# Kernel tuning notes

Hardware: AMD Instinct MI355X
Metric: run time of the kernel (lower is better)

Reference implementation:

```python
import jax, jax.numpy as jnp
import numpy as np

N_HEADS = 16


def setup_inputs() -> dict:
    key = jax.random.key(0)
    ks = jax.random.split(key, 9)
    B, T, C, S = 32, 8, 1024, 4096
    w_scale = 1.0 / np.sqrt(C).astype(np.float32)
    return {
        "x": jax.random.normal(ks[0], (B, T, C), jnp.float32),
        "cache_k": jax.random.normal(ks[1], (B, S, C), jnp.float32),
        "cache_v": jax.random.normal(ks[2], (B, S, C), jnp.float32),
        "cache_len": jax.random.randint(ks[3], (B,), 0, S - T, jnp.int32),
        "wq": jax.random.normal(ks[4], (C, C), jnp.float32) * w_scale,
        "wk": jax.random.normal(ks[5], (C, C), jnp.float32) * w_scale,
        "wv": jax.random.normal(ks[6], (C, C), jnp.float32) * w_scale,
        "wo": jax.random.normal(ks[7], (C, C), jnp.float32) * w_scale,
        "bo": jnp.zeros((C,), jnp.float32),
    }


def reference(x, cache_k, cache_v, cache_len, wq, wk, wv, wo, bo):
    # Decode step with KV cache (use_cache=True, window_size=None, mask=None).
    B, T, C = x.shape
    S = cache_k.shape[1]  # max_seq_len (static pad; torch pads to max(cache_len))
    H = N_HEADS
    hd = C // H

    # Projections (torch Linear: y = x @ W^T)
    q = x @ wq.T
    k_new = x @ wk.T
    v_new = x @ wv.T

    # Ragged past-KV gather: zero-pad each row beyond its cache_len,
    # exactly like the per-batch loop + padded_k/padded_v in torch.
    pos = jnp.arange(S)
    past_mask = (pos[None, :] < cache_len[:, None])[..., None]  # (B, S, 1)
    past_k = jnp.where(past_mask, cache_k, 0.0)
    past_v = jnp.where(past_mask, cache_v, 0.0)

    k = jnp.concatenate([past_k, k_new], axis=1)  # (B, S+T, C)
    v = jnp.concatenate([past_v, v_new], axis=1)

    def to_heads(t):
        return t.reshape(B, t.shape[1], H, hd).transpose(0, 2, 1, 3)

    qh, kh, vh = to_heads(q), to_heads(k), to_heads(v)  # (B,H,*,hd)

    scores = jnp.einsum('bhqd,bhkd->bhqk', qh, kh) / np.sqrt(hd).astype(np.float32)

    # Torch only materializes keys up to max(cache_len); slots beyond that
    # do not exist there, so mask them out. Slots in [cache_len_b, max_cl)
    # are zero-padded keys (score 0, value 0) in torch -> kept as-is here.
    max_cl = jnp.max(cache_len)
    key_valid = jnp.concatenate([pos < max_cl, jnp.ones((T,), bool)])  # (S+T,)
    NEG = jnp.float32(-1e30)
    scores = jnp.where(key_valid[None, None, None, :], scores, NEG)

    attn = jax.nn.softmax(scores, axis=-1)
    out = jnp.einsum('bhqk,bhkd->bhqd', attn, vh)
    out = out.transpose(0, 2, 1, 3).reshape(B, T, C)
    return out @ wo.T + bo
```

## Files before the change

### kernel.cpp

```cpp
#include <hip/hip_runtime.h>

constexpr int Bn = 32, Tn = 8, Cn = 1024, Sn = 4096, Hn = 16, HDn = 64;
constexpr int CHUNK = 64, NCHUNK = 64;
constexpr int KSPLIT = 4;
constexpr float SCALE = 0.125f;

constexpr size_t PROJ_PART = (size_t)Bn * Tn * Cn;
constexpr size_t QP_OFF = 0;
constexpr size_t KP_OFF = QP_OFF + KSPLIT * PROJ_PART;
constexpr size_t VP_OFF = KP_OFF + KSPLIT * PROJ_PART;
constexpr size_t PACC_OFF = VP_OFF + KSPLIT * PROJ_PART;
constexpr size_t PACC_SZ = (size_t)NCHUNK * Bn * Hn * Tn * HDn;
constexpr size_t PL_OFF = PACC_OFF + PACC_SZ;
constexpr size_t PL_SZ = (size_t)NCHUNK * Bn * Hn * Tn;
constexpr size_t AW_OFF = PL_OFF + PL_SZ;
constexpr size_t AW_SZ = PROJ_PART;
constexpr size_t OP_OFF = AW_OFF + AW_SZ;
constexpr size_t OP_SZ = (size_t)KSPLIT * PROJ_PART;
constexpr size_t QR_OFF = OP_OFF + OP_SZ;
constexpr size_t KN_OFF = QR_OFF + PROJ_PART;
constexpr size_t VN_OFF = KN_OFF + PROJ_PART;

typedef __attribute__((address_space(3))) unsigned int lds_uint;
typedef const __attribute__((address_space(1))) unsigned int glb_uint;

__device__ __forceinline__ void gload_lds16(const float* g, float* l) {
    __builtin_amdgcn_global_load_lds((glb_uint*)g, (lds_uint*)l, 16, 0, 0);
}

__device__ __forceinline__ void gemm_body(const float* __restrict__ X,
                                          const float* __restrict__ W,
                                          float* __restrict__ Opart,
                                          int sigma, int jblk, int iblk) {
    __shared__ float wl[64][68];
    const int tid = threadIdx.x;
    const int c = tid & 15, a = tid >> 4;
    const int j0 = jblk * 64;
    const int ib = iblk * 64 + a * 4;
    const int k0 = sigma * 256;

    float acc[4][4];
#pragma unroll
    for (int ii = 0; ii < 4; ++ii)
#pragma unroll
        for (int jj = 0; jj < 4; ++jj) acc[ii][jj] = 0.f;

    for (int kt = 0; kt < 4; ++kt) {
        const int k1 = k0 + kt * 64;
#pragma unroll
        for (int stp = 0; stp < 4; ++stp) {
            int f4 = stp * 256 + tid;
            int jr = f4 >> 4, e4 = f4 & 15;
            float4 wv = *(const float4*)&W[(size_t)(j0 + jr) * Cn + k1 + e4 * 4];
            wl[e4 * 4 + 0][jr] = wv.x;
            wl[e4 * 4 + 1][jr] = wv.y;
            wl[e4 * 4 + 2][jr] = wv.z;
            wl[e4 * 4 + 3][jr] = wv.w;
        }
        __syncthreads();
#pragma unroll 4
        for (int k4 = 0; k4 < 16; ++k4) {
            float4 xv[4];
#pragma unroll
            for (int ii = 0; ii < 4; ++ii)
                xv[ii] = *(const float4*)&X[(size_t)(ib + ii) * Cn + k1 + k4 * 4];
#pragma unroll
            for (int kk = 0; kk < 4; ++kk) {
                float4 wv = *(const float4*)&wl[k4 * 4 + kk][c * 4];
#pragma unroll
                for (int ii = 0; ii < 4; ++ii) {
                    const float xs = (kk == 0) ? xv[ii].x : (kk == 1) ? xv[ii].y
                                   : (kk == 2) ? xv[ii].z : xv[ii].w;
                    acc[ii][0] += xs * wv.x;
                    acc[ii][1] += xs * wv.y;
                    acc[ii][2] += xs * wv.z;
                    acc[ii][3] += xs * wv.w;
                }
            }
        }
        __syncthreads();
    }
    float* op = Opart + (size_t)sigma * PROJ_PART;
#pragma unroll
    for (int ii = 0; ii < 4; ++ii) {
        float4 o = make_float4(acc[ii][0], acc[ii][1], acc[ii][2], acc[ii][3]);
        *(float4*)&op[(size_t)(ib + ii) * Cn + j0 + c * 4] = o;
    }
}

__global__ __launch_bounds__(256) void proj3_kernel(
    const float* __restrict__ X, const float* __restrict__ W0,
    const float* __restrict__ W1, const float* __restrict__ W2,
    float* __restrict__ O0, float* __restrict__ O1, float* __restrict__ O2) {
    const int z = blockIdx.z;
    const float* W = (z < 4) ? W0 : (z < 8 ? W1 : W2);
    float* O = (z < 4) ? O0 : (z < 8 ? O1 : O2);
    gemm_body(X, W, O, z & 3, blockIdx.x, blockIdx.y);
}

__global__ __launch_bounds__(256) void gemm1_kernel(
    const float* __restrict__ X, const float* __restrict__ W, float* __restrict__ O) {
    gemm_body(X, W, O, blockIdx.z, blockIdx.x, blockIdx.y);
}

__global__ __launch_bounds__(256) void prereduce_kernel(
    const float* __restrict__ qp, const float* __restrict__ kp,
    const float* __restrict__ vp, float* __restrict__ q,
    float* __restrict__ kn, float* __restrict__ vn) {
    const size_t i = ((size_t)blockIdx.x * 256 + threadIdx.x) * 4;
#define SUM4(P)                                                              \
    make_float4(                                                             \
        (*(const float4*)(P + i)).x + (*(const float4*)(P + PROJ_PART + i)).x + \
        (*(const float4*)(P + 2 * PROJ_PART + i)).x + (*(const float4*)(P + 3 * PROJ_PART + i)).x, \
        (*(const float4*)(P + i)).y + (*(const float4*)(P + PROJ_PART + i)).y + \
        (*(const float4*)(P + 2 * PROJ_PART + i)).y + (*(const float4*)(P + 3 * PROJ_PART + i)).y, \
        (*(const float4*)(P + i)).z + (*(const float4*)(P + PROJ_PART + i)).z + \
        (*(const float4*)(P + 2 * PROJ_PART + i)).z + (*(const float4*)(P + 3 * PROJ_PART + i)).z, \
        (*(const float4*)(P + i)).w + (*(const float4*)(P + PROJ_PART + i)).w + \
        (*(const float4*)(P + 2 * PROJ_PART + i)).w + (*(const float4*)(P + 3 * PROJ_PART + i)).w)
    float4 qv = SUM4(qp);
    qv.x *= SCALE; qv.y *= SCALE; qv.z *= SCALE; qv.w *= SCALE;
    *(float4*)&q[i] = qv;
    *(float4*)&kn[i] = SUM4(kp);
    *(float4*)&vn[i] = SUM4(vp);
#undef SUM4
}

__global__ __launch_bounds__(64) void attn_kernel(
    const float* __restrict__ q, const float* __restrict__ kn,
    const float* __restrict__ vn, const float* __restrict__ ck,
    const float* __restrict__ cv, const int* __restrict__ clen,
    float* __restrict__ pacc, float* __restrict__ pl) {
    const int h = blockIdx.x, cq = blockIdx.y, b = blockIdx.z;
    const int cl = clen[b];
    if (cq != 0 && cq * CHUNK >= cl) return;

    const int lane = threadIdx.x;
    const int rg = lane >> 4;
    const int slot = lane & 15;
    const int swz = lane & 15;

    __shared__ float K_l[64][64];
    __shared__ float q_l[8][64];
    __shared__ float p_l[8][64];

    int mv = clen[lane & 31];
#pragma unroll
    for (int off = 16; off >= 1; off >>= 1) {
        int o = __shfl_xor(mv, off);
        mv = mv > o ? mv : o;
    }

    {
        const float* qb0 = q + (size_t)b * Tn * Cn + (size_t)h * HDn;
#pragma unroll
        for (int i = 0; i < 2; ++i) {
            const int row = i * 4 + rg;
            gload_lds16(qb0 + (size_t)row * Cn + slot * 4, &q_l[i * 4][0]);
        }
    }
    const size_t gb = ((size_t)b * Sn + (size_t)cq * CHUNK) * Cn + (size_t)h * HDn;
#pragma unroll
    for (int i = 0; i < 16; ++i) {
        const int row = i * 4 + rg;
        gload_lds16(ck + gb + (size_t)row * Cn + (slot ^ (row & 15)) * 4, &K_l[i * 4][0]);
    }
    __builtin_amdgcn_sched_barrier(0);
    const float* vb = cv + gb + lane;
    float vq0[16];
#pragma unroll
    for (int r = 0; r < 16; ++r) vq0[r] = vb[(size_t)r * Cn];
    __builtin_amdgcn_sched_barrier(0);

    const int nv = min(max(cl - cq * CHUNK, 0), CHUNK);

    asm volatile("s_waitcnt vmcnt(16)" ::: "memory");
    __builtin_amdgcn_sched_barrier(0);

    float s[8];
#pragma unroll
    for (int t = 0; t < 8; ++t) s[t] = 0.f;
#pragma unroll
    for (int dg = 0; dg < 16; ++dg) {
        const float4 kv = *(const float4*)&K_l[lane][(dg ^ swz) * 4];
#pragma unroll
        for (int t = 0; t < 8; ++t) {
            const float4 qv = *(const float4*)&q_l[t][dg * 4];
            s[t] += kv.x * qv.x + kv.y * qv.y + kv.z * qv.z + kv.w * qv.w;
        }
    }
    const bool val = lane < nv;
    float lden[8];
#pragma unroll
    for (int t = 0; t < 8; ++t) {
        const float p = val ? __expf(s[t]) : 0.f;
        lden[t] = p;
        p_l[t][lane] = p;
    }

    float av[8];
#pragma unroll
    for (int t = 0; t < 8; ++t) av[t] = 0.f;

#define PVQ(VQ, BASE)                                                         \
    do {                                                                      \
        _Pragma("unroll")                                                     \
        for (int r4 = 0; r4 < 4; ++r4) {                                      \
            float4 pt[8];                                                     \
            _Pragma("unroll")                                                 \
            for (int t = 0; t < 8; ++t)                                       \
                pt[t] = *(const float4*)&p_l[t][(BASE) + r4 * 4];             \
            _Pragma("unroll")                                                 \
            for (int u = 0; u < 4; ++u) {                                     \
                const float v = VQ[r4 * 4 + u];                               \
                _Pragma("unroll")                                             \
                for (int t = 0; t < 8; ++t) {                                 \
                    const float pu = (u == 0) ? pt[t].x                       \
                                   : (u == 1) ? pt[t].y                       \
                                   : (u == 2) ? pt[t].z : pt[t].w;            \
                    av[t] += pu * v;                                          \
                }                                                             \
            }                                                                 \
        }                                                                     \
    } while (0)

    float vq1[16];
#pragma unroll
    for (int r = 0; r < 16; ++r) vq1[r] = vb[(size_t)(16 + r) * Cn];
    PVQ(vq0, 0);
    float vq2[16];
#pragma unroll
    for (int r = 0; r < 16; ++r) vq2[r] = vb[(size_t)(32 + r) * Cn];
    PVQ(vq1, 16);
    float vq3[16];
#pragma unroll
    for (int r = 0; r < 16; ++r) vq3[r] = vb[(size_t)(48 + r) * Cn];
    PVQ(vq2, 32);
    PVQ(vq3, 48);
#undef PVQ

    if (cq == 0) {
        const int r = lane >> 3, dgrp = lane & 7;
        const float* kb = kn + ((size_t)b * Tn + r) * Cn + (size_t)h * HDn + dgrp * 8;
        const float4 ka = *(const float4*)(kb);
        const float4 kc = *(const float4*)(kb + 4);
        float sn[8];
#pragma unroll
        for (int t = 0; t < 8; ++t) {
            const float4 qa = *(const float4*)&q_l[t][dgrp * 8];
            const float4 qc = *(const float4*)&q_l[t][dgrp * 8 + 4];
            float v = ka.x * qa.x + ka.y * qa.y + ka.z * qa.z + ka.w * qa.w +
                      kc.x * qc.x + kc.y * qc.y + kc.z * qc.z + kc.w * qc.w;
            v += __shfl_xor(v, 1);
            v += __shfl_xor(v, 2);
            v += __shfl_xor(v, 4);
            sn[t] = v;
        }
        if (dgrp == 0) {
#pragma unroll
            for (int t = 0; t < 8; ++t) {
                const float p = __expf(sn[t]);
                p_l[t][r] = p;
                lden[t] += p;
            }
        }
        const float* vb2 = vn + (size_t)b * Tn * Cn + (size_t)h * HDn + lane;
#pragma unroll
        for (int r2 = 0; r2 < 8; ++r2) {
            const float v = vb2[(size_t)r2 * Cn];
#pragma unroll
            for (int t = 0; t < 8; ++t) av[t] += p_l[t][r2] * v;
        }
    }

#pragma unroll
    for (int t = 0; t < 8; ++t) {
        float v = lden[t];
#pragma unroll
        for (int off = 32; off >= 1; off >>= 1) v += __shfl_xor(v, off);
        lden[t] = v;
    }
    if (cq == 0) {
        const float pad = (float)(mv - cl);
#pragma unroll
        for (int t = 0; t < 8; ++t) lden[t] += pad;
    }

    const size_t obase = (size_t)((cq * Bn + b) * Hn + h);
#pragma unroll
    for (int t = 0; t < 8; ++t) pacc[obase * 512 + (size_t)t * 64 + lane] = av[t];
    if (lane == 0) {
#pragma unroll
        for (int t = 0; t < 8; ++t) pl[obase * 8 + t] = lden[t];
    }
}

__global__ __launch_bounds__(256) void attn_merge_kernel(
    const float* __restrict__ pacc, const float* __restrict__ pl,
    const int* __restrict__ clen, float* __restrict__ aw) {
    const int h = blockIdx.x, b = blockIdx.y;
    const int tid = threadIdx.x, wave = tid >> 6, lane = tid & 63;
    const int cl = clen[b];
    int nch = (cl + CHUNK - 1) / CHUNK;
    if (nch < 1) nch = 1;

    __shared__ float racc[4][8][64];
    __shared__ float rl[4][8];

    float acc[8], l[8];
#pragma unroll
    for (int t = 0; t < 8; ++t) { acc[t] = 0.f; l[t] = 0.f; }
    for (int c = wave; c < nch; c += 4) {
        const size_t base = (size_t)((c * Bn + b) * Hn + h);
#pragma unroll
        for (int t = 0; t < 8; ++t) acc[t] += pacc[base * 512 + t * 64 + lane];
#pragma unroll
        for (int t = 0; t < 8; ++t) l[t] += pl[base * 8 + t];
    }
#pragma unroll
    for (int t = 0; t < 8; ++t) racc[wave][t][lane] = acc[t];
    if (lane == 0) {
#pragma unroll
        for (int t = 0; t < 8; ++t) rl[wave][t] = l[t];
    }
    __syncthreads();
#pragma unroll
    for (int rep = 0; rep < 2; ++rep) {
        const int e = rep * 256 + tid;
        const int t = e >> 6, d = e & 63;
        const float a = racc[0][t][d] + racc[1][t][d] + racc[2][t][d] + racc[3][t][d];
        const float ll = rl[0][t] + rl[1][t] + rl[2][t] + rl[3][t];
        aw[(size_t)(b * Tn + t) * Cn + (size_t)h * HDn + d] = a / ll;
    }
}

__global__ __launch_bounds__(256) void bias_out_kernel(
    const float* __restrict__ opart, const float* __restrict__ bo, float* __restrict__ out) {
    const int f4 = blockIdx.x * 256 + threadIdx.x;
    const float4 a0 = *(const float4*)(opart + (size_t)f4 * 4);
    const float4 a1 = *(const float4*)(opart + PROJ_PART + (size_t)f4 * 4);
    const float4 a2 = *(const float4*)(opart + 2 * PROJ_PART + (size_t)f4 * 4);
    const float4 a3 = *(const float4*)(opart + 3 * PROJ_PART + (size_t)f4 * 4);
    const float4 bv = *(const float4*)&bo[(f4 & 255) * 4];
    float4 o = make_float4(a0.x + a1.x + a2.x + a3.x + bv.x,
                           a0.y + a1.y + a2.y + a3.y + bv.y,
                           a0.z + a1.z + a2.z + a3.z + bv.z,
                           a0.w + a1.w + a2.w + a3.w + bv.w);
    *(float4*)&out[(size_t)f4 * 4] = o;
}

extern "C" void kernel_launch(void* const* d_in, const int* in_sizes, int n_in,
                              void* d_out, int out_size, void* d_ws, size_t ws_size,
                              hipStream_t stream) {
    const float* x  = (const float*)d_in[0];
    const float* ck = (const float*)d_in[1];
    const float* cv = (const float*)d_in[2];
    const int*   cl = (const int*)d_in[3];
    const float* wq = (const float*)d_in[4];
    const float* wk = (const float*)d_in[5];
    const float* wv = (const float*)d_in[6];
    const float* wo = (const float*)d_in[7];
    const float* bo = (const float*)d_in[8];
    float* out = (float*)d_out;
    float* ws = (float*)d_ws;

    float* qpart = ws + QP_OFF;
    float* kpart = ws + KP_OFF;
    float* vpart = ws + VP_OFF;
    float* pacc  = ws + PACC_OFF;
    float* pl    = ws + PL_OFF;
    float* aw    = ws + AW_OFF;
    float* opart = ws + OP_OFF;
    float* qr    = ws + QR_OFF;
    float* knew  = ws + KN_OFF;
    float* vnew  = ws + VN_OFF;

    proj3_kernel<<<dim3(16, 4, 12), dim3(256), 0, stream>>>(x, wq, wk, wv, qpart, kpart, vpart);
    prereduce_kernel<<<dim3(256), dim3(256), 0, stream>>>(qpart, kpart, vpart, qr, knew, vnew);
    attn_kernel<<<dim3(Hn, NCHUNK, Bn), dim3(64), 0, stream>>>(qr, knew, vnew, ck, cv, cl, pacc, pl);
    attn_merge_kernel<<<dim3(Hn, Bn), dim3(256), 0, stream>>>(pacc, pl, cl, aw);
    gemm1_kernel<<<dim3(16, 4, KSPLIT), dim3(256), 0, stream>>>(aw, wo, opart);
    bias_out_kernel<<<dim3(256), dim3(256), 0, stream>>>(opart, bo, out);
}
```

Measured before the change: 204.1 us.

## Process 256-key chunks per block with an inner 64-key loop and K prefetch

Each attention block now covers 256 cache positions instead of 64, iterating over four 64-key sub-tiles. It accumulates the softmax denominators and PV products in registers and prefetches the next K tile into LDS while doing the PV work of the current one. This cuts the number of partial-result chunks written and later reduced by 4x and amortises per-block setup such as the q load and the max-length reduction. In exchange there are 4x fewer blocks, so less parallelism across the GPU, and a longer serial dependency inside each block. Reusing the K LDS buffer while lanes may still be reading it is also a hazard, since there is no barrier.

```diff
diff --git a/kernel.cpp b/kernel.cpp
--- a/kernel.cpp
+++ b/kernel.cpp
@@ -1,7 +1,7 @@
 #include <hip/hip_runtime.h>
 
 constexpr int Bn = 32, Tn = 8, Cn = 1024, Sn = 4096, Hn = 16, HDn = 64;
-constexpr int CHUNK = 64, NCHUNK = 64;
+constexpr int CHUNK = 256, NCHUNK = 16;
 constexpr int KSPLIT = 4;
 constexpr float SCALE = 0.125f;
 
@@ -151,6 +151,9 @@
         mv = mv > o ? mv : o;
     }
 
+    const int nv = min(max(cl - cq * CHUNK, 0), CHUNK);
+    const int nst = (nv + 63) >> 6;
+
     {
         const float* qb0 = q + (size_t)b * Tn * Cn + (size_t)h * HDn;
 #pragma unroll
@@ -160,47 +163,58 @@
         }
     }
     const size_t gb = ((size_t)b * Sn + (size_t)cq * CHUNK) * Cn + (size_t)h * HDn;
-#pragma unroll
-    for (int i = 0; i < 16; ++i) {
-        const int row = i * 4 + rg;
-        gload_lds16(ck + gb + (size_t)row * Cn + (slot ^ (row & 15)) * 4, &K_l[i * 4][0]);
-    }
-    __builtin_amdgcn_sched_barrier(0);
-    const float* vb = cv + gb + lane;
-    float vq0[16];
-#pragma unroll
-    for (int r = 0; r < 16; ++r) vq0[r] = vb[(size_t)r * Cn];
-    __builtin_amdgcn_sched_barrier(0);
-
-    const int nv = min(max(cl - cq * CHUNK, 0), CHUNK);
-
-    asm volatile("s_waitcnt vmcnt(16)" ::: "memory");
-    __builtin_amdgcn_sched_barrier(0);
-
-    float s[8];
-#pragma unroll
-    for (int t = 0; t < 8; ++t) s[t] = 0.f;
-#pragma unroll
-    for (int dg = 0; dg < 16; ++dg) {
-        const float4 kv = *(const float4*)&K_l[lane][(dg ^ swz) * 4];
+
+    auto issueK = [&](int s) {
+#pragma unroll
+        for (int i = 0; i < 16; ++i) {
+            const int row = i * 4 + rg;
+            gload_lds16(ck + gb + (size_t)(s * 64 + row) * Cn + (slot ^ (row & 15)) * 4,
+                        &K_l[i * 4][0]);
+        }
+    };
+
+    float av[8], lden[8];
+#pragma unroll
+    for (int t = 0; t < 8; ++t) { av[t] = 0.f; lden[t] = 0.f; }
+
+    if (nst > 0) {
+        issueK(0);
+        __builtin_amdgcn_sched_barrier(0);
+    }
+
+    for (int s = 0; s < nst; ++s) {
+        const float* vb = cv + gb + (size_t)s * 64 * Cn + lane;
+        float vq0[16];
+#pragma unroll
+        for (int r = 0; r < 16; ++r) vq0[r] = vb[(size_t)r * Cn];
+        __builtin_amdgcn_sched_barrier(0);
+        asm volatile("s_waitcnt vmcnt(16)" ::: "memory");
+        __builtin_amdgcn_sched_barrier(0);
+
+        float sc[8];
+#pragma unroll
+        for (int t = 0; t < 8; ++t) sc[t] = 0.f;
+#pragma unroll
+        for (int dg = 0; dg < 16; ++dg) {
+            const float4 kv = *(const float4*)&K_l[lane][(dg ^ swz) * 4];
+#pragma unroll
+            for (int t = 0; t < 8; ++t) {
+                const float4 qv = *(const float4*)&q_l[t][dg * 4];
+                sc[t] += kv.x * qv.x + kv.y * qv.y + kv.z * qv.z + kv.w * qv.w;
+            }
+        }
+        const bool val = lane < nv - s * 64;
 #pragma unroll
         for (int t = 0; t < 8; ++t) {
-            const float4 qv = *(const float4*)&q_l[t][dg * 4];
-            s[t] += kv.x * qv.x + kv.y * qv.y + kv.z * qv.z + kv.w * qv.w;
-        }
-    }
-    const bool val = lane < nv;
-    float lden[8];
-#pragma unroll
-    for (int t = 0; t < 8; ++t) {
-        const float p = val ? __expf(s[t]) : 0.f;
-        lden[t] = p;
-        p_l[t][lane] = p;
-    }
-
-    float av[8];
-#pragma unroll
-    for (int t = 0; t < 8; ++t) av[t] = 0.f;
+            const float p = val ? __expf(sc[t]) : 0.f;
+            lden[t] += p;
+            p_l[t][lane] = p;
+        }
+        __builtin_amdgcn_sched_barrier(0);
+        if (s + 1 < nst) {
+            issueK(s + 1);
+            __builtin_amdgcn_sched_barrier(0);
+        }
 
 #define PVQ(VQ, BASE)                                                         \
     do {                                                                      \
@@ -224,20 +238,21 @@
         }                                                                     \
     } while (0)
 
-    float vq1[16];
-#pragma unroll
-    for (int r = 0; r < 16; ++r) vq1[r] = vb[(size_t)(16 + r) * Cn];
-    PVQ(vq0, 0);
-    float vq2[16];
-#pragma unroll
-    for (int r = 0; r < 16; ++r) vq2[r] = vb[(size_t)(32 + r) * Cn];
-    PVQ(vq1, 16);
-    float vq3[16];
-#pragma unroll
-    for (int r = 0; r < 16; ++r) vq3[r] = vb[(size_t)(48 + r) * Cn];
-    PVQ(vq2, 32);
-    PVQ(vq3, 48);
+        float vq1[16];
+#pragma unroll
+        for (int r = 0; r < 16; ++r) vq1[r] = vb[(size_t)(16 + r) * Cn];
+        PVQ(vq0, 0);
+        float vq2[16];
+#pragma unroll
+        for (int r = 0; r < 16; ++r) vq2[r] = vb[(size_t)(32 + r) * Cn];
+        PVQ(vq1, 16);
+        float vq3[16];
+#pragma unroll
+        for (int r = 0; r < 16; ++r) vq3[r] = vb[(size_t)(48 + r) * Cn];
+        PVQ(vq2, 32);
+        PVQ(vq3, 48);
 #undef PVQ
+    }
 
     if (cq == 0) {
         const int r = lane >> 3, dgrp = lane & 7;
```

New measurement: 269.4 us. 32.0% more time.

## Process two heads per attention block and prefetch second head's K/V

Applied to the files above, without the earlier changes.

Each attention workgroup now handles a pair of heads (h and h+8) instead of one, halving the grid's head dimension. After the first head's QK scores are computed, the second head's K tile is issued into the reused LDS buffer and its first V rows into registers. These loads overlap with the first head's PV accumulation, hiding memory latency within a single wave. The cost is fewer workgroups for latency hiding and higher register pressure from holding extra V prefetch registers.

```diff
diff --git a/kernel.cpp b/kernel.cpp
--- a/kernel.cpp
+++ b/kernel.cpp
@@ -131,7 +131,8 @@
     const float* __restrict__ vn, const float* __restrict__ ck,
     const float* __restrict__ cv, const int* __restrict__ clen,
     float* __restrict__ pacc, float* __restrict__ pl) {
-    const int h = blockIdx.x, cq = blockIdx.y, b = blockIdx.z;
+    const int hA = blockIdx.x, hB = hA + 8;
+    const int cq = blockIdx.y, b = blockIdx.z;
     const int cl = clen[b];
     if (cq != 0 && cq * CHUNK >= cl) return;
 
@@ -141,7 +142,7 @@
     const int swz = lane & 15;
 
     __shared__ float K_l[64][64];
-    __shared__ float q_l[8][64];
+    __shared__ float q_l[2][8][64];
     __shared__ float p_l[8][64];
 
     int mv = clen[lane & 31];
@@ -151,72 +152,70 @@
         mv = mv > o ? mv : o;
     }
 
-    {
-        const float* qb0 = q + (size_t)b * Tn * Cn + (size_t)h * HDn;
-#pragma unroll
-        for (int i = 0; i < 2; ++i) {
-            const int row = i * 4 + rg;
-            gload_lds16(qb0 + (size_t)row * Cn + slot * 4, &q_l[i * 4][0]);
-        }
-    }
-    const size_t gb = ((size_t)b * Sn + (size_t)cq * CHUNK) * Cn + (size_t)h * HDn;
+    const int nv = min(max(cl - cq * CHUNK, 0), CHUNK);
+
+    const float* qbase = q + (size_t)b * Tn * Cn;
+#pragma unroll
+    for (int i = 0; i < 2; ++i) {
+        const int row = i * 4 + rg;
+        gload_lds16(qbase + (size_t)row * Cn + hA * HDn + slot * 4, &q_l[0][i * 4][0]);
+    }
+#pragma unroll
+    for (int i = 0; i < 2; ++i) {
+        const int row = i * 4 + rg;
+        gload_lds16(qbase + (size_t)row * Cn + hB * HDn + slot * 4, &q_l[1][i * 4][0]);
+    }
+    __builtin_amdgcn_sched_barrier(0);
+    const size_t gbA = ((size_t)b * Sn + (size_t)cq * CHUNK) * Cn + (size_t)hA * HDn;
+    const size_t gbB = ((size_t)b * Sn + (size_t)cq * CHUNK) * Cn + (size_t)hB * HDn;
 #pragma unroll
     for (int i = 0; i < 16; ++i) {
         const int row = i * 4 + rg;
-        gload_lds16(ck + gb + (size_t)row * Cn + (slot ^ (row & 15)) * 4, &K_l[i * 4][0]);
-    }
-    __builtin_amdgcn_sched_barrier(0);
-    const float* vb = cv + gb + lane;
+        gload_lds16(ck + gbA + (size_t)row * Cn + (slot ^ (row & 15)) * 4, &K_l[i * 4][0]);
+    }
+    __builtin_amdgcn_sched_barrier(0);
+    const float* vbA = cv + gbA + lane;
     float vq0[16];
 #pragma unroll
-    for (int r = 0; r < 16; ++r) vq0[r] = vb[(size_t)r * Cn];
-    __builtin_amdgcn_sched_barrier(0);
-
-    const int nv = min(max(cl - cq * CHUNK, 0), CHUNK);
+    for (int r = 0; r < 16; ++r) vq0[r] = vbA[(size_t)r * Cn];
+    __builtin_amdgcn_sched_barrier(0);
+
+    float av[8], lden[8];
+#pragma unroll
+    for (int t = 0; t < 8; ++t) { av[t] = 0.f; lden[t] = 0.f; }
 
     asm volatile("s_waitcnt vmcnt(16)" ::: "memory");
     __builtin_amdgcn_sched_barrier(0);
 
-    float s[8];
-#pragma unroll
-    for (int t = 0; t < 8; ++t) s[t] = 0.f;
-#pragma unroll
-    for (int dg = 0; dg < 16; ++dg) {
-        const float4 kv = *(const float4*)&K_l[lane][(dg ^ swz) * 4];
-#pragma unroll
-        for (int t = 0; t < 8; ++t) {
-            const float4 qv = *(const float4*)&q_l[t][dg * 4];
-            s[t] += kv.x * qv.x + kv.y * qv.y + kv.z * qv.z + kv.w * qv.w;
-        }
-    }
-    const bool val = lane < nv;
-    float lden[8];
-#pragma unroll
-    for (int t = 0; t < 8; ++t) {
-        const float p = val ? __expf(s[t]) : 0.f;
-        lden[t] = p;
-        p_l[t][lane] = p;
-    }
-
-    float av[8];
-#pragma unroll
-    for (int t = 0; t < 8; ++t) av[t] = 0.f;
+#define QK_PHASE(QI)                                                          \
+    do {                                                                      \
+        float sc[8];                                                          \
+        _Pragma("unroll") for (int t = 0; t < 8; ++t) sc[t] = 0.f;            \
+        _Pragma("unroll") for (int dg = 0; dg < 16; ++dg) {                   \
+            const float4 kv = *(const float4*)&K_l[lane][(dg ^ swz) * 4];     \
+            _Pragma("unroll") for (int t = 0; t < 8; ++t) {                   \
+                const float4 qv = *(const float4*)&q_l[QI][t][dg * 4];        \
+                sc[t] += kv.x * qv.x + kv.y * qv.y + kv.z * qv.z + kv.w * qv.w; \
+            }                                                                 \
+        }                                                                     \
+        const bool val = lane < nv;                                           \
+        _Pragma("unroll") for (int t = 0; t < 8; ++t) {                       \
+            const float p = val ? __expf(sc[t]) : 0.f;                        \
+            lden[t] += p;                                                     \
+            p_l[t][lane] = p;                                                 \
+        }                                                                     \
+    } while (0)
 
 #define PVQ(VQ, BASE)                                                         \
     do {                                                                      \
-        _Pragma("unroll")                                                     \
-        for (int r4 = 0; r4 < 4; ++r4) {                                      \
+        _Pragma("unroll") for (int r4 = 0; r4 < 4; ++r4) {                    \
             float4 pt[8];                                                     \
-            _Pragma("unroll")                                                 \
-            for (int t = 0; t < 8; ++t)                                       \
+            _Pragma("unroll") for (int t = 0; t < 8; ++t)                     \
                 pt[t] = *(const float4*)&p_l[t][(BASE) + r4 * 4];             \
-            _Pragma("unroll")                                                 \
-            for (int u = 0; u < 4; ++u) {                                     \
+            _Pragma("unroll") for (int u = 0; u < 4; ++u) {                   \
                 const float v = VQ[r4 * 4 + u];                               \
-                _Pragma("unroll")                                             \
-                for (int t = 0; t < 8; ++t) {                                 \
-                    const float pu = (u == 0) ? pt[t].x                       \
-                                   : (u == 1) ? pt[t].y                       \
+                _Pragma("unroll") for (int t = 0; t < 8; ++t) {               \
+                    const float pu = (u == 0) ? pt[t].x : (u == 1) ? pt[t].y  \
                                    : (u == 2) ? pt[t].z : pt[t].w;            \
                     av[t] += pu * v;                                          \
                 }                                                             \
@@ -224,75 +223,120 @@
         }                                                                     \
     } while (0)
 
-    float vq1[16];
-#pragma unroll
-    for (int r = 0; r < 16; ++r) vq1[r] = vb[(size_t)(16 + r) * Cn];
-    PVQ(vq0, 0);
-    float vq2[16];
-#pragma unroll
-    for (int r = 0; r < 16; ++r) vq2[r] = vb[(size_t)(32 + r) * Cn];
-    PVQ(vq1, 16);
-    float vq3[16];
-#pragma unroll
-    for (int r = 0; r < 16; ++r) vq3[r] = vb[(size_t)(48 + r) * Cn];
-    PVQ(vq2, 32);
-    PVQ(vq3, 48);
+#define NEWKEYS(QI, H)                                                        \
+    do {                                                                      \
+        const int r = lane >> 3, dgrp = lane & 7;                             \
+        const float* kb = kn + ((size_t)b * Tn + r) * Cn + (size_t)(H) * HDn + dgrp * 8; \
+        const float4 ka = *(const float4*)(kb);                               \
+        const float4 kc = *(const float4*)(kb + 4);                           \
+        float sn[8];                                                          \
+        _Pragma("unroll") for (int t = 0; t < 8; ++t) {                       \
+            const float4 qa = *(const float4*)&q_l[QI][t][dgrp * 8];          \
+            const float4 qc = *(const float4*)&q_l[QI][t][dgrp * 8 + 4];      \
+            float v = ka.x * qa.x + ka.y * qa.y + ka.z * qa.z + ka.w * qa.w + \
+                      kc.x * qc.x + kc.y * qc.y + kc.z * qc.z + kc.w * qc.w;  \
+            v += __shfl_xor(v, 1);                                            \
+            v += __shfl_xor(v, 2);                                            \
+            v += __shfl_xor(v, 4);                                            \
+            sn[t] = v;                                                        \
+        }                                                                     \
+        if (dgrp == 0) {                                                      \
+            _Pragma("unroll") for (int t = 0; t < 8; ++t) {                   \
+                const float p = __expf(sn[t]);                                \
+                p_l[t][r] = p;                                                \
+                lden[t] += p;                                                 \
+            }                                                                 \
+        }                                                                     \
+        const float* vb2 = vn + (size_t)b * Tn * Cn + (size_t)(H) * HDn + lane; \
+        _Pragma("unroll") for (int r2 = 0; r2 < 8; ++r2) {                    \
+            const float v = vb2[(size_t)r2 * Cn];                             \
+            _Pragma("unroll") for (int t = 0; t < 8; ++t)                     \
+                av[t] += p_l[t][r2] * v;                                      \
+        }                                                                     \
+    } while (0)
+
+#define EPILOGUE(H)                                                           \
+    do {                                                                      \
+        _Pragma("unroll") for (int t = 0; t < 8; ++t) {                       \
+            float v = lden[t];                                                \
+            _Pragma("unroll") for (int off = 32; off >= 1; off >>= 1)         \
+                v += __shfl_xor(v, off);                                      \
+            lden[t] = v;                                                      \
+        }                                                                     \
+        if (cq == 0) {                                                        \
+            const float pad = (float)(mv - cl);                               \
+            _Pragma("unroll") for (int t = 0; t < 8; ++t) lden[t] += pad;     \
+        }                                                                     \
+        const size_t obase = (size_t)((cq * Bn + b) * Hn + (H));              \
+        _Pragma("unroll") for (int t = 0; t < 8; ++t)                         \
+            pacc[obase * 512 + (size_t)t * 64 + lane] = av[t];                \
+        if (lane == 0) {                                                      \
+            _Pragma("unroll") for (int t = 0; t < 8; ++t)                     \
+                pl[obase * 8 + t] = lden[t];                                  \
+        }                                                                     \
+    } while (0)
+
+    QK_PHASE(0);
+    __builtin_amdgcn_sched_barrier(0);
+#pragma unroll
+    for (int i = 0; i < 16; ++i) {
+        const int row = i * 4 + rg;
+        gload_lds16(ck + gbB + (size_t)row * Cn + (slot ^ (row & 15)) * 4, &K_l[i * 4][0]);
+    }
+    __builtin_amdgcn_sched_barrier(0);
+    const float* vbB = cv + gbB + lane;
+    float vqB0[16];
+#pragma unroll
+    for (int r = 0; r < 16; ++r) vqB0[r] = vbB[(size_t)r * Cn];
+    __builtin_amdgcn_sched_barrier(0);
+
+    {
+        float vq1[16];
+#pragma unroll
+        for (int r = 0; r < 16; ++r) vq1[r] = vbA[(size_t)(16 + r) * Cn];
+        PVQ(vq0, 0);
+        float vq2[16];
+#pragma unroll
+        for (int r = 0; r < 16; ++r) vq2[r] = vbA[(size_t)(32 + r) * Cn];
+        PVQ(vq1, 16);
+        float vq3[16];
+#pragma unroll
+        for (int r = 0; r < 16; ++r) vq3[r] = vbA[(size_t)(48 + r) * Cn];
+        PVQ(vq2, 32);
+        PVQ(vq3, 48);
+    }
+    if (cq == 0) NEWKEYS(0, hA);
+    EPILOGUE(hA);
+
+#pragma unroll
+    for (int t = 0; t < 8; ++t) { av[t] = 0.f; lden[t] = 0.f; }
+    asm volatile("s_waitcnt vmcnt(0)" ::: "memory");
+    __builtin_amdgcn_sched_barrier(0);
+
+    QK_PHASE(1);
+    __builtin_amdgcn_sched_barrier(0);
+    {
+        float vq1[16];
+#pragma unroll
+        for (int r = 0; r < 16; ++r) vq1[r] = vbB[(size_t)(16 + r) * Cn];
+        PVQ(vqB0, 0);
+        float vq2[16];
+#pragma unroll
+        for (int r = 0; r < 16; ++r) vq2[r] = vbB[(size_t)(32 + r) * Cn];
+        PVQ(vq1, 16);
+        float vq3[16];
+#pragma unroll
+        for (int r = 0; r < 16; ++r) vq3[r] = vbB[(size_t)(48 + r) * Cn];
+        PVQ(vq2, 32);
+        PVQ(vq3, 48);
+    }
+    if (cq == 0) NEWKEYS(1, hB);
+    EPILOGUE(hB);
+
+#undef QK_PHASE
 #undef PVQ
-
-    if (cq == 0) {
-        const int r = lane >> 3, dgrp = lane & 7;
-        const float* kb = kn + ((size_t)b * Tn + r) * Cn + (size_t)h * HDn + dgrp * 8;
-        const float4 ka = *(const float4*)(kb);
-        const float4 kc = *(const float4*)(kb + 4);
-        float sn[8];
-#pragma unroll
-        for (int t = 0; t < 8; ++t) {
-            const float4 qa = *(const float4*)&q_l[t][dgrp * 8];
-            const float4 qc = *(const float4*)&q_l[t][dgrp * 8 + 4];
-            float v = ka.x * qa.x + ka.y * qa.y + ka.z * qa.z + ka.w * qa.w +
-                      kc.x * qc.x + kc.y * qc.y + kc.z * qc.z + kc.w * qc.w;
-            v += __shfl_xor(v, 1);
-            v += __shfl_xor(v, 2);
-            v += __shfl_xor(v, 4);
-            sn[t] = v;
-        }
-        if (dgrp == 0) {
-#pragma unroll
-            for (int t = 0; t < 8; ++t) {
-                const float p = __expf(sn[t]);
-                p_l[t][r] = p;
-                lden[t] += p;
-            }
-        }
-        const float* vb2 = vn + (size_t)b * Tn * Cn + (size_t)h * HDn + lane;
-#pragma unroll
-        for (int r2 = 0; r2 < 8; ++r2) {
-            const float v = vb2[(size_t)r2 * Cn];
-#pragma unroll
-            for (int t = 0; t < 8; ++t) av[t] += p_l[t][r2] * v;
-        }
-    }
-
-#pragma unroll
-    for (int t = 0; t < 8; ++t) {
-        float v = lden[t];
-#pragma unroll
-        for (int off = 32; off >= 1; off >>= 1) v += __shfl_xor(v, off);
-        lden[t] = v;
-    }
-    if (cq == 0) {
-        const float pad = (float)(mv - cl);
-#pragma unroll
-        for (int t = 0; t < 8; ++t) lden[t] += pad;
-    }
-
-    const size_t obase = (size_t)((cq * Bn + b) * Hn + h);
-#pragma unroll
-    for (int t = 0; t < 8; ++t) pacc[obase * 512 + (size_t)t * 64 + lane] = av[t];
-    if (lane == 0) {
-#pragma unroll
-        for (int t = 0; t < 8; ++t) pl[obase * 8 + t] = lden[t];
-    }
+#undef NEWKEYS
+#undef EPILOGUE
 }
 
 __global__ __launch_bounds__(256) void attn_merge_kernel(
@@ -377,7 +421,7 @@
 
     proj3_kernel<<<dim3(16, 4, 12), dim3(256), 0, stream>>>(x, wq, wk, wv, qpart, kpart, vpart);
     prereduce_kernel<<<dim3(256), dim3(256), 0, stream>>>(qpart, kpart, vpart, qr, knew, vnew);
-    attn_kernel<<<dim3(Hn, NCHUNK, Bn), dim3(64), 0, stream>>>(qr, knew, vnew, ck, cv, cl, pacc, pl);
+    attn_kernel<<<dim3(8, NCHUNK, Bn), dim3(64), 0, stream>>>(qr, knew, vnew, ck, cv, cl, pacc, pl);
     attn_merge_kernel<<<dim3(Hn, Bn), dim3(256), 0, stream>>>(pacc, pl, cl, aw);
     gemm1_kernel<<<dim3(16, 4, KSPLIT), dim3(256), 0, stream>>>(aw, wo, opart);
     bias_out_kernel<<<dim3(256), dim3(256), 0, stream>>>(opart, bo, out);
```

After: 219.4 us. 7.5% more time.

## Broadcast q and probabilities via readlane instead of LDS in attention kernel

Applied to the files above, without the earlier changes.

The attention kernel keeps q and the softmax probabilities in per-lane registers and broadcasts them with v_readlane instead of staging them in LDS arrays. Chunk loads are skipped when the chunk has no valid keys. The new-token K path reuses the K LDS buffer and computes its scores the same way. This removes LDS traffic and shuffle reductions, but readlane is a scalar-pipe operation, and the many readlanes in the QK and PV loops may serialize and cost more than the LDS reads they replace.

```diff
diff --git a/kernel.cpp b/kernel.cpp
--- a/kernel.cpp
+++ b/kernel.cpp
@@ -26,6 +26,10 @@
 
 __device__ __forceinline__ void gload_lds16(const float* g, float* l) {
     __builtin_amdgcn_global_load_lds((glb_uint*)g, (lds_uint*)l, 16, 0, 0);
+}
+
+__device__ __forceinline__ float rlf(float v, int l) {
+    return __uint_as_float((unsigned)__builtin_amdgcn_readlane((int)__float_as_uint(v), l));
 }
 
 __device__ __forceinline__ void gemm_body(const float* __restrict__ X,
@@ -141,8 +145,6 @@
     const int swz = lane & 15;
 
     __shared__ float K_l[64][64];
-    __shared__ float q_l[8][64];
-    __shared__ float p_l[8][64];
 
     int mv = clen[lane & 31];
 #pragma unroll
@@ -151,139 +153,132 @@
         mv = mv > o ? mv : o;
     }
 
+    float qreg[8];
     {
-        const float* qb0 = q + (size_t)b * Tn * Cn + (size_t)h * HDn;
-#pragma unroll
+        const float* qb = q + (size_t)b * Tn * Cn + (size_t)h * HDn + lane;
+#pragma unroll
+        for (int t = 0; t < 8; ++t) qreg[t] = qb[(size_t)t * Cn];
+    }
+
+    const int nv = min(max(cl - cq * CHUNK, 0), CHUNK);
+    const size_t gb = ((size_t)b * Sn + (size_t)cq * CHUNK) * Cn + (size_t)h * HDn;
+
+    float av[8], lden8[8], p[8];
+#pragma unroll
+    for (int t = 0; t < 8; ++t) { av[t] = 0.f; lden8[t] = 0.f; p[t] = 0.f; }
+
+    if (nv > 0) {
+#pragma unroll
+        for (int i = 0; i < 16; ++i) {
+            const int row = i * 4 + rg;
+            gload_lds16(ck + gb + (size_t)row * Cn + (slot ^ (row & 15)) * 4,
+                        &K_l[i * 4][0]);
+        }
+        __builtin_amdgcn_sched_barrier(0);
+        const float* vb = cv + gb + lane;
+        float vq0[16];
+#pragma unroll
+        for (int r = 0; r < 16; ++r) vq0[r] = vb[(size_t)r * Cn];
+        __builtin_amdgcn_sched_barrier(0);
+
+        asm volatile("s_waitcnt vmcnt(16)" ::: "memory");
+        __builtin_amdgcn_sched_barrier(0);
+
+        float sc[8];
+#pragma unroll
+        for (int t = 0; t < 8; ++t) sc[t] = 0.f;
+#pragma unroll
+        for (int dg = 0; dg < 16; ++dg) {
+            const float4 kv = *(const float4*)&K_l[lane][(dg ^ swz) * 4];
+#pragma unroll
+            for (int t = 0; t < 8; ++t) {
+                sc[t] += kv.x * rlf(qreg[t], dg * 4 + 0);
+                sc[t] += kv.y * rlf(qreg[t], dg * 4 + 1);
+                sc[t] += kv.z * rlf(qreg[t], dg * 4 + 2);
+                sc[t] += kv.w * rlf(qreg[t], dg * 4 + 3);
+            }
+        }
+        const bool val = lane < nv;
+#pragma unroll
+        for (int t = 0; t < 8; ++t) {
+            p[t] = val ? __expf(sc[t]) : 0.f;
+            lden8[t] += p[t];
+        }
+
+#define PVQ(VQ, BASE)                                                         \
+    do {                                                                      \
+        _Pragma("unroll") for (int r = 0; r < 16; ++r) {                      \
+            const float v = VQ[r];                                            \
+            _Pragma("unroll") for (int t = 0; t < 8; ++t)                     \
+                av[t] += rlf(p[t], (BASE) + r) * v;                           \
+        }                                                                     \
+    } while (0)
+
+        float vq1[16];
+#pragma unroll
+        for (int r = 0; r < 16; ++r) vq1[r] = vb[(size_t)(16 + r) * Cn];
+        PVQ(vq0, 0);
+        float vq2[16];
+#pragma unroll
+        for (int r = 0; r < 16; ++r) vq2[r] = vb[(size_t)(32 + r) * Cn];
+        PVQ(vq1, 16);
+        float vq3[16];
+#pragma unroll
+        for (int r = 0; r < 16; ++r) vq3[r] = vb[(size_t)(48 + r) * Cn];
+        PVQ(vq2, 32);
+        PVQ(vq3, 48);
+#undef PVQ
+    }
+
+    if (cq == 0) {
         for (int i = 0; i < 2; ++i) {
             const int row = i * 4 + rg;
-            gload_lds16(qb0 + (size_t)row * Cn + slot * 4, &q_l[i * 4][0]);
-        }
-    }
-    const size_t gb = ((size_t)b * Sn + (size_t)cq * CHUNK) * Cn + (size_t)h * HDn;
-#pragma unroll
-    for (int i = 0; i < 16; ++i) {
-        const int row = i * 4 + rg;
-        gload_lds16(ck + gb + (size_t)row * Cn + (slot ^ (row & 15)) * 4, &K_l[i * 4][0]);
-    }
-    __builtin_amdgcn_sched_barrier(0);
-    const float* vb = cv + gb + lane;
-    float vq0[16];
-#pragma unroll
-    for (int r = 0; r < 16; ++r) vq0[r] = vb[(size_t)r * Cn];
-    __builtin_amdgcn_sched_barrier(0);
-
-    const int nv = min(max(cl - cq * CHUNK, 0), CHUNK);
-
-    asm volatile("s_waitcnt vmcnt(16)" ::: "memory");
-    __builtin_amdgcn_sched_barrier(0);
-
-    float s[8];
-#pragma unroll
-    for (int t = 0; t < 8; ++t) s[t] = 0.f;
-#pragma unroll
-    for (int dg = 0; dg < 16; ++dg) {
-        const float4 kv = *(const float4*)&K_l[lane][(dg ^ swz) * 4];
+            gload_lds16(kn + ((size_t)b * Tn + row) * Cn + (size_t)h * HDn +
+                            (slot ^ row) * 4,
+                        &K_l[i * 4][0]);
+        }
+        asm volatile("s_waitcnt vmcnt(0)" ::: "memory");
+        __builtin_amdgcn_sched_barrier(0);
+
+        const int rown = lane & 7;
+        float sn[8];
+#pragma unroll
+        for (int t = 0; t < 8; ++t) sn[t] = 0.f;
+        for (int dg = 0; dg < 16; ++dg) {
+            const float4 kv = *(const float4*)&K_l[rown][(dg ^ rown) * 4];
+#pragma unroll
+            for (int t = 0; t < 8; ++t) {
+                sn[t] += kv.x * rlf(qreg[t], dg * 4 + 0);
+                sn[t] += kv.y * rlf(qreg[t], dg * 4 + 1);
+                sn[t] += kv.z * rlf(qreg[t], dg * 4 + 2);
+                sn[t] += kv.w * rlf(qreg[t], dg * 4 + 3);
+            }
+        }
+        float pn[8];
 #pragma unroll
         for (int t = 0; t < 8; ++t) {
-            const float4 qv = *(const float4*)&q_l[t][dg * 4];
-            s[t] += kv.x * qv.x + kv.y * qv.y + kv.z * qv.z + kv.w * qv.w;
-        }
-    }
-    const bool val = lane < nv;
-    float lden[8];
+            pn[t] = (lane < 8) ? __expf(sn[t]) : 0.f;
+            lden8[t] += pn[t];
+        }
+        const float* vb2 = vn + (size_t)b * Tn * Cn + (size_t)h * HDn + lane;
+        for (int r = 0; r < 8; ++r) {
+            const float v = vb2[(size_t)r * Cn];
+#pragma unroll
+            for (int t = 0; t < 8; ++t) av[t] += rlf(pn[t], r) * v;
+        }
+    }
+
 #pragma unroll
     for (int t = 0; t < 8; ++t) {
-        const float p = val ? __expf(s[t]) : 0.f;
-        lden[t] = p;
-        p_l[t][lane] = p;
-    }
-
-    float av[8];
-#pragma unroll
-    for (int t = 0; t < 8; ++t) av[t] = 0.f;
-
-#define PVQ(VQ, BASE)                                                         \
-    do {                                                                      \
-        _Pragma("unroll")                                                     \
-        for (int r4 = 0; r4 < 4; ++r4) {                                      \
-            float4 pt[8];                                                     \
-            _Pragma("unroll")                                                 \
-            for (int t = 0; t < 8; ++t)                                       \
-                pt[t] = *(const float4*)&p_l[t][(BASE) + r4 * 4];             \
-            _Pragma("unroll")                                                 \
-            for (int u = 0; u < 4; ++u) {                                     \
-                const float v = VQ[r4 * 4 + u];                               \
-                _Pragma("unroll")                                             \
-                for (int t = 0; t < 8; ++t) {                                 \
-                    const float pu = (u == 0) ? pt[t].x                       \
-                                   : (u == 1) ? pt[t].y                       \
-                                   : (u == 2) ? pt[t].z : pt[t].w;            \
-                    av[t] += pu * v;                                          \
-                }                                                             \
-            }                                                                 \
-        }                                                                     \
-    } while (0)
-
-    float vq1[16];
-#pragma unroll
-    for (int r = 0; r < 16; ++r) vq1[r] = vb[(size_t)(16 + r) * Cn];
-    PVQ(vq0, 0);
-    float vq2[16];
-#pragma unroll
-    for (int r = 0; r < 16; ++r) vq2[r] = vb[(size_t)(32 + r) * Cn];
-    PVQ(vq1, 16);
-    float vq3[16];
-#pragma unroll
-    for (int r = 0; r < 16; ++r) vq3[r] = vb[(size_t)(48 + r) * Cn];
-    PVQ(vq2, 32);
-    PVQ(vq3, 48);
-#undef PVQ
-
-    if (cq == 0) {
-        const int r = lane >> 3, dgrp = lane & 7;
-        const float* kb = kn + ((size_t)b * Tn + r) * Cn + (size_t)h * HDn + dgrp * 8;
-        const float4 ka = *(const float4*)(kb);
-        const float4 kc = *(const float4*)(kb + 4);
-        float sn[8];
-#pragma unroll
-        for (int t = 0; t < 8; ++t) {
-            const float4 qa = *(const float4*)&q_l[t][dgrp * 8];
-            const float4 qc = *(const float4*)&q_l[t][dgrp * 8 + 4];
-            float v = ka.x * qa.x + ka.y * qa.y + ka.z * qa.z + ka.w * qa.w +
-                      kc.x * qc.x + kc.y * qc.y + kc.z * qc.z + kc.w * qc.w;
-            v += __shfl_xor(v, 1);
-            v += __shfl_xor(v, 2);
-            v += __shfl_xor(v, 4);
-            sn[t] = v;
-        }
-        if (dgrp == 0) {
-#pragma unroll
-            for (int t = 0; t < 8; ++t) {
-                const float p = __expf(sn[t]);
-                p_l[t][r] = p;
-                lden[t] += p;
-            }
-        }
-        const float* vb2 = vn + (size_t)b * Tn * Cn + (size_t)h * HDn + lane;
-#pragma unroll
-        for (int r2 = 0; r2 < 8; ++r2) {
-            const float v = vb2[(size_t)r2 * Cn];
-#pragma unroll
-            for (int t = 0; t < 8; ++t) av[t] += p_l[t][r2] * v;
-        }
-    }
-
-#pragma unroll
-    for (int t = 0; t < 8; ++t) {
-        float v = lden[t];
+        float v = lden8[t];
 #pragma unroll
         for (int off = 32; off >= 1; off >>= 1) v += __shfl_xor(v, off);
-        lden[t] = v;
+        lden8[t] = v;
     }
     if (cq == 0) {
         const float pad = (float)(mv - cl);
 #pragma unroll
-        for (int t = 0; t < 8; ++t) lden[t] += pad;
+        for (int t = 0; t < 8; ++t) lden8[t] += pad;
     }
 
     const size_t obase = (size_t)((cq * Bn + b) * Hn + h);
@@ -291,7 +286,7 @@
     for (int t = 0; t < 8; ++t) pacc[obase * 512 + (size_t)t * 64 + lane] = av[t];
     if (lane == 0) {
 #pragma unroll
-        for (int t = 0; t < 8; ++t) pl[obase * 8 + t] = lden[t];
+        for (int t = 0; t < 8; ++t) pl[obase * 8 + t] = lden8[t];
     }
 }
 
```

Result: no change. 207.6 us (+1.7%).
